# Optimization experiments

Measured on AMD Instinct MI355X. Metric: run time of the kernel, lower is better.

Reference implementation:

```python
import jax, jax.numpy as jnp
import numpy as np

K = 7          # kernel_size
PAD = 3        # padding
GROUPS = 8
OUTC = 128
INC = 128
REFINE = True


def conv1x1(x, w):
    # x: [B,C,H,W], w: [O,C] (1x1 conv, no bias)
    return jnp.einsum('oc,bchw->bohw', w, x)


def unfold2d(x, k):
    # x: [B,C,Hp,Wp] -> [B,C,h,w,k,k], stride 1 (matches torch unfold(2,k).unfold(3,k))
    B, C, Hp, Wp = x.shape
    h, w = Hp - k + 1, Wp - k + 1
    patches = jnp.stack([x[:, :, i:i + h, j:j + w] for i in range(k) for j in range(k)], axis=-1)
    return patches.reshape(B, C, h, w, k, k)


def unfold1d(x, k, axis):
    # sliding window of size k, stride 1, along axis 2 (rows) or 3 (cols)
    if axis == 2:
        h = x.shape[2] - k + 1
        return jnp.stack([x[:, :, i:i + h, :] for i in range(k)], axis=-1)  # [B,C,h,W,k]
    else:
        w = x.shape[3] - k + 1
        return jnp.stack([x[:, :, :, j:j + w] for j in range(k)], axis=-1)  # [B,C,H,w,k]


def _forward(feature_map, wq, wk, wv, rel_h, rel_w):
    c = feature_map.shape[1] // 2
    fm_t0, fm_t1 = feature_map[:, :c], feature_map[:, c:]
    B, _, H, W = fm_t0.shape
    cg = OUTC // GROUPS

    padded_t0 = jnp.pad(fm_t0, ((0, 0), (0, 0), (PAD, PAD), (PAD, PAD)))
    q = conv1x1(fm_t1, wq)                 # [B,OUTC,H,W]
    k_full = conv1x1(padded_t0, wk)        # [B,OUTC,H+2p,W+2p]
    v_full = conv1x1(padded_t0, wv)

    k_win = unfold2d(k_full, K)            # [B,OUTC,H,W,K,K]
    k_h, k_w = k_win[:, :OUTC // 2], k_win[:, OUTC // 2:]
    k_win = jnp.concatenate([k_h + rel_h, k_w + rel_w], axis=1)
    k_win = k_win.reshape(B, GROUPS, cg, H, W, K * K)
    v_win = unfold2d(v_full, K).reshape(B, GROUPS, cg, H, W, K * K)

    qg = q.reshape(B, GROUPS, cg, H, W, 1)
    attn = jax.nn.softmax(jnp.sum(qg * k_win, axis=2), axis=-1)  # [B,G,H,W,K*K]
    out = jnp.einsum('bnhwk,bnchwk->bnchw', attn, v_win).reshape(B, OUTC, H, W)

    if REFINE:
        win = 2 * K + 1
        p_col = jnp.pad(fm_t0, ((0, 0), (0, 0), (K, K), (0, 0)))
        p_row = jnp.pad(fm_t0, ((0, 0), (0, 0), (0, 0), (K, K)))
        k_col = unfold1d(conv1x1(p_col, wk), win, 2).reshape(B, GROUPS, cg, H, W, win)
        k_row = unfold1d(conv1x1(p_row, wk), win, 3).reshape(B, GROUPS, cg, H, W, win)
        v_col = unfold1d(conv1x1(p_col, wv), win, 2).reshape(B, GROUPS, cg, H, W, win)
        v_row = unfold1d(conv1x1(p_row, wv), win, 3).reshape(B, GROUPS, cg, H, W, win)

        a_row = jax.nn.softmax(jnp.sum(qg * k_row, axis=2), axis=-1)
        a_col = jax.nn.softmax(jnp.sum(qg * k_col, axis=2), axis=-1)
        out = out + jnp.einsum('bnhwk,bnchwk->bnchw', a_row, v_row).reshape(B, OUTC, H, W)
        out = out + jnp.einsum('bnhwk,bnchwk->bnchw', a_col, v_col).reshape(B, OUTC, H, W)
    return out


def setup_inputs() -> dict:
    key = jax.random.key(0)
    ks = jax.random.split(key, 6)
    B, H, W = 2, 64, 64
    feature_map = jax.random.normal(ks[0], (B, 2 * INC, H, W), dtype=jnp.float32)
    # kaiming_normal fan_out for 1x1 conv: std = sqrt(2 / outc)
    std = float(np.sqrt(2.0 / OUTC))
    wq = jax.random.normal(ks[1], (OUTC, INC), dtype=jnp.float32) * std
    wk = jax.random.normal(ks[2], (OUTC, INC), dtype=jnp.float32) * std
    wv = jax.random.normal(ks[3], (OUTC, INC), dtype=jnp.float32) * std
    rel_h = jax.random.normal(ks[4], (OUTC // 2, 1, 1, K, 1), dtype=jnp.float32)
    rel_w = jax.random.normal(ks[5], (OUTC // 2, 1, 1, 1, K), dtype=jnp.float32)
    return {"feature_map": feature_map, "wq": wq, "wk": wk, "wv": wv,
            "rel_h": rel_h, "rel_w": rel_w}


def reference(feature_map, wq, wk, wv, rel_h, rel_w):
    return _forward(feature_map, wq, wk, wv, rel_h, rel_w)
```

## Files before the change

### kernel.cpp

```cpp
#include <hip/hip_runtime.h>
#include <hip/hip_bf16.h>

__device__ __forceinline__ float bf2f(unsigned short u) {
    union { unsigned int i; float f; } v; v.i = ((unsigned int)u) << 16; return v.f;
}
__device__ __forceinline__ unsigned short f2bf(float f) {
    __hip_bfloat16 h = __float2bfloat16(f);
    return *reinterpret_cast<unsigned short*>(&h);
}


#define CANVAS_SLAB 102400

__device__ __forceinline__ void zero_pad_slice(
    unsigned short* __restrict__ C, int blockId, int tid)
{
    const int slab = blockId >> 4;
    const int part = blockId & 15;
    unsigned short* base = C + (size_t)slab * CANVAS_SLAB;
    #pragma unroll
    for (int r = 0; r < 2; ++r) {
        const int t = tid + r * 256;
        if (t < 288) {
            const int u    = part * 288 + t;
            const int cell = u >> 1;
            const int half = u & 1;
            int row, col;
            if (cell < 640)       { row = cell / 80;  col = cell - row * 80; }
            else if (cell < 1280) { const int c2 = cell - 640;  const int rr = c2 / 80;
                                    row = 72 + rr;  col = c2 - rr * 80; }
            else if (cell < 1792) { const int c2 = cell - 1280;
                                    row = 8 + (c2 >> 3);  col = c2 & 7; }
            else                  { const int c2 = cell - 1792;
                                    row = 8 + (c2 >> 3);  col = 72 + (c2 & 7); }
            *(uint4*)(base + (size_t)(row * 80 + col) * 16 + half * 8) =
                make_uint4(0u, 0u, 0u, 0u);
        }
    }
}

__global__ __launch_bounds__(256) void conv_kernel(
    const float* __restrict__ fm,
    const float* __restrict__ wq, const float* __restrict__ wk,
    const float* __restrict__ wv,
    float* __restrict__ Qout,
    unsigned short* __restrict__ K0,
    unsigned short* __restrict__ V0)
{
    const int sel = blockIdx.z;
    const int by  = blockIdx.y;
    const float* W = (sel == 0) ? wq : ((sel == 1) ? wk : wv);
    const int c0 = (sel == 0) ? 128 : 0;

    __shared__ float w_s[64 * 68];
    __shared__ float x_s[64 * 68];

    const int tid = threadIdx.x;
    const int P0  = blockIdx.x * 64;
    const int b   = P0 >> 12;
    const int hw0 = P0 & 4095;

    if (sel == 1) zero_pad_slice(K0, blockIdx.x * 2 + by, tid);
    else if (sel == 2) zero_pad_slice(V0, blockIdx.x * 2 + by, tid);

    float acc[4][4];
    #pragma unroll
    for (int i = 0; i < 4; ++i)
        #pragma unroll
        for (int j = 0; j < 4; ++j) acc[i][j] = 0.f;

    const int ocb = (tid >> 4) * 4;
    const int pxb = (tid & 15) * 4;

    for (int kh = 0; kh < 128; kh += 64) {
        {
            const int o    = tid >> 2;
            const int koff = (tid & 3) * 16;
            #pragma unroll
            for (int i = 0; i < 4; ++i) {
                float4 v = *(const float4*)(W + (size_t)(by * 64 + o) * 128 + kh + koff + i * 4);
                w_s[(koff + i * 4 + 0) * 68 + o] = v.x;
                w_s[(koff + i * 4 + 1) * 68 + o] = v.y;
                w_s[(koff + i * 4 + 2) * 68 + o] = v.z;
                w_s[(koff + i * 4 + 3) * 68 + o] = v.w;
            }
        }
        {
            const int c  = tid >> 2;
            const int pc = (tid & 3) * 16;
            const float* src = fm + (((size_t)(b * 256 + c0 + kh + c)) << 12) + hw0 + pc;
            #pragma unroll
            for (int i = 0; i < 4; ++i)
                *(float4*)(&x_s[c * 68 + pc + i * 4]) = *(const float4*)(src + i * 4);
        }
        __syncthreads();
        #pragma unroll 8
        for (int k = 0; k < 64; ++k) {
            float4 wa = *(const float4*)(&w_s[k * 68 + ocb]);
            float4 xv = *(const float4*)(&x_s[k * 68 + pxb]);
            const float wf[4] = {wa.x, wa.y, wa.z, wa.w};
            const float xf[4] = {xv.x, xv.y, xv.z, xv.w};
            #pragma unroll
            for (int i = 0; i < 4; ++i)
                #pragma unroll
                for (int j = 0; j < 4; ++j) acc[i][j] += wf[i] * xf[j];
        }
        __syncthreads();
    }

    const int oc  = by * 64 + ocb;
    const int g   = oc >> 4;
    const int lci = oc & 15;
    const int hh  = hw0 >> 6;
    #pragma unroll
    for (int pj = 0; pj < 4; ++pj) {
        const int ww = pxb + pj;
        if (sel == 0) {
            const size_t base = ((((size_t)(b * 8 + g)) << 12) + (hh * 64 + ww)) * 16 + lci;
            *(float4*)(Qout + base) = make_float4(acc[0][pj], acc[1][pj], acc[2][pj], acc[3][pj]);
        } else {
            const size_t cbase = (size_t)(b * 8 + g) * CANVAS_SLAB
                               + ((size_t)((hh + 8) * 80 + (ww + 8))) * 16 + lci;
            unsigned short tmp[4];
            #pragma unroll
            for (int i = 0; i < 4; ++i) tmp[i] = f2bf(acc[i][pj]);
            unsigned short* dst = ((sel == 1) ? K0 : V0) + cbase;
            *(uint2*)dst = *(const uint2*)tmp;
        }
    }
}

struct KV16 { uint4 a, b; };
__device__ __forceinline__ KV16 ld16(const unsigned short* p) {
    KV16 r; r.a = *(const uint4*)p; r.b = *(const uint4*)(p + 8); return r;
}
__device__ __forceinline__ float dotq(const float* q, const KV16& k) {
    const unsigned short* u = (const unsigned short*)&k;
    float s = 0.f;
    #pragma unroll
    for (int c = 0; c < 16; ++c) s += q[c] * bf2f(u[c]);
    return s;
}
__device__ __forceinline__ void axpyq(float* acc, float wgt, const KV16& v) {
    const unsigned short* u = (const unsigned short*)&v;
    #pragma unroll
    for (int c = 0; c < 16; ++c) acc[c] += wgt * bf2f(u[c]);
}

#define CIDX(y, x) (((size_t)(((y) + 8) * 80 + ((x) + 8))) << 4)

template<int I0, int NI>
__device__ __forceinline__ void main_chunk(
    const float* qr, const unsigned short* Kp, const unsigned short* Vp,
    const float* __restrict__ rel_h, const float* __restrict__ rel_w,
    int g, int h, int w, float* acc, float& mx, float& den)
{
    float qrel[7];
    const float* rel = (g < 4) ? (rel_h + g * 112) : (rel_w + (g - 4) * 112);
    #pragma unroll
    for (int t = 0; t < 7; ++t) {
        float s = 0.f;
        #pragma unroll
        for (int ci = 0; ci < 16; ++ci) s += qr[ci] * rel[ci * 7 + t];
        qrel[t] = s;
    }
    const bool bias_i = (g < 4);

    float sc[NI * 7];
    mx = -3.4e38f;
    #pragma unroll
    for (int i = 0; i < NI; ++i) {
        const int y = h + (I0 + i) - 3;
        #pragma unroll
        for (int j = 0; j < 7; ++j) {
            const int x = w + j - 3;
            float d = dotq(qr, ld16(Kp + CIDX(y, x)));
            d += bias_i ? qrel[I0 + i] : qrel[j];
            sc[i * 7 + j] = d;
            mx = fmaxf(mx, d);
        }
    }
    den = 0.f;
    #pragma unroll
    for (int k = 0; k < NI * 7; ++k) { sc[k] = __expf(sc[k] - mx); den += sc[k]; }
    #pragma unroll
    for (int i = 0; i < NI; ++i) {
        const int y = h + (I0 + i) - 3;
        #pragma unroll
        for (int j = 0; j < 7; ++j) {
            const int x = w + j - 3;
            axpyq(acc, sc[i * 7 + j], ld16(Vp + CIDX(y, x)));
        }
    }
}

__global__ __launch_bounds__(256) void attn_kernel(
    const float* __restrict__ Q,
    const unsigned short* __restrict__ K0,
    const unsigned short* __restrict__ V0,
    const float* __restrict__ rel_h,
    const float* __restrict__ rel_w,
    float* __restrict__ ACC,
    float* __restrict__ Mb,
    float* __restrict__ Db)
{
    const int tid = threadIdx.x;
    const int id  = blockIdx.x;
    const int s   = id & 15;
    const int j   = id >> 4;
    const int xt  = j & 15;
    const int pz  = j >> 4;
    const int b   = s >> 3;
    const int g   = s & 7;
    const int w   = tid & 63;
    const int h   = xt * 4 + (tid >> 6);

    const size_t slabQ = ((size_t)s) << 16;
    const float* qptr = Q + slabQ + (size_t)(h * 64 + w) * 16;

    float qr[16];
    #pragma unroll
    for (int ci = 0; ci < 16; ++ci) qr[ci] = qptr[ci];

    const unsigned short* Kp = K0 + (size_t)s * CANVAS_SLAB;
    const unsigned short* Vp = V0 + (size_t)s * CANVAS_SLAB;

    float acc[16];
    #pragma unroll
    for (int ci = 0; ci < 16; ++ci) acc[ci] = 0.f;
    float mx, den;

    if (pz == 0) {
        main_chunk<4, 3>(qr, Kp, Vp, rel_h, rel_w, g, h, w, acc, mx, den);
    } else if (pz == 1) {
        main_chunk<0, 2>(qr, Kp, Vp, rel_h, rel_w, g, h, w, acc, mx, den);
    } else if (pz == 2) {
        main_chunk<2, 2>(qr, Kp, Vp, rel_h, rel_w, g, h, w, acc, mx, den);
    } else if (pz == 3) {
        float sc[15];
        mx = -3.4e38f;
        #pragma unroll
        for (int jj = 0; jj < 15; ++jj) {
            const int x = w + jj - 7;
            const float d = dotq(qr, ld16(Kp + CIDX(h, x)));
            sc[jj] = d; mx = fmaxf(mx, d);
        }
        den = 0.f;
        #pragma unroll
        for (int jj = 0; jj < 15; ++jj) { sc[jj] = __expf(sc[jj] - mx); den += sc[jj]; }
        #pragma unroll
        for (int jj = 0; jj < 15; ++jj) {
            const int x = w + jj - 7;
            axpyq(acc, sc[jj], ld16(Vp + CIDX(h, x)));
        }
    } else {
        float sc[15];
        mx = -3.4e38f;
        #pragma unroll
        for (int i = 0; i < 15; ++i) {
            const int y = h + i - 7;
            const float d = dotq(qr, ld16(Kp + CIDX(y, w)));
            sc[i] = d; mx = fmaxf(mx, d);
        }
        den = 0.f;
        #pragma unroll
        for (int i = 0; i < 15; ++i) { sc[i] = __expf(sc[i] - mx); den += sc[i]; }
        #pragma unroll
        for (int i = 0; i < 15; ++i) {
            const int y = h + i - 7;
            axpyq(acc, sc[i], ld16(Vp + CIDX(y, w)));
        }
    }

    const int hw = h * 64 + w;
    float* op = ACC + ((((size_t)(pz * 2 + b)) * 128 + g * 16) << 12) + hw;
    #pragma unroll
    for (int ci = 0; ci < 16; ++ci)
        op[(size_t)ci << 12] = acc[ci];
    const size_t md = ((((size_t)(pz * 2 + b)) * 8 + g) << 12) + hw;
    Mb[md] = mx;
    Db[md] = den;
}
#undef CIDX

__global__ __launch_bounds__(256) void combine_kernel(
    const float4* __restrict__ ACC,
    const float* __restrict__ Mb, const float* __restrict__ Db,
    float4* __restrict__ out)
{
    const int idx = blockIdx.x * 256 + threadIdx.x;
    const int i4  = idx & 1023;
    const int ch  = (idx >> 10) & 127;
    const int b   = idx >> 17;
    const int g   = ch >> 4;

    const float4* M4 = (const float4*)Mb;
    const float4* D4 = (const float4*)Db;

    float4 A[5], Mv[3], Dv[5];
    #pragma unroll
    for (int p = 0; p < 5; ++p) {
        A[p]  = ACC[(((size_t)(p * 2 + b) * 128 + ch) << 10) + i4];
        Dv[p] = D4[(((size_t)(p * 2 + b) * 8 + g) << 10) + i4];
    }
    #pragma unroll
    for (int p = 0; p < 3; ++p)
        Mv[p] = M4[(((size_t)(p * 2 + b) * 8 + g) << 10) + i4];

    const float* a0 = (const float*)&A[0]; const float* a1 = (const float*)&A[1];
    const float* a2 = (const float*)&A[2]; const float* a3 = (const float*)&A[3];
    const float* a4 = (const float*)&A[4];
    const float* m0 = (const float*)&Mv[0]; const float* m1 = (const float*)&Mv[1];
    const float* m2 = (const float*)&Mv[2];
    const float* d0 = (const float*)&Dv[0]; const float* d1 = (const float*)&Dv[1];
    const float* d2 = (const float*)&Dv[2]; const float* d3 = (const float*)&Dv[3];
    const float* d4 = (const float*)&Dv[4];

    float res[4];
    #pragma unroll
    for (int c = 0; c < 4; ++c) {
        const float M  = fmaxf(m0[c], fmaxf(m1[c], m2[c]));
        const float e0 = __expf(m0[c] - M);
        const float e1 = __expf(m1[c] - M);
        const float e2 = __expf(m2[c] - M);
        const float num = a0[c] * e0 + a1[c] * e1 + a2[c] * e2;
        const float den = d0[c] * e0 + d1[c] * e1 + d2[c] * e2;
        res[c] = num / den + a3[c] / d3[c] + a4[c] / d4[c];
    }
    out[idx] = make_float4(res[0], res[1], res[2], res[3]);
}

extern "C" void kernel_launch(void* const* d_in, const int* in_sizes, int n_in,
                              void* d_out, int out_size, void* d_ws, size_t ws_size,
                              hipStream_t stream) {
    (void)in_sizes; (void)n_in; (void)ws_size; (void)out_size;
    const float* fm    = (const float*)d_in[0];
    const float* wq    = (const float*)d_in[1];
    const float* wk    = (const float*)d_in[2];
    const float* wv    = (const float*)d_in[3];
    const float* rel_h = (const float*)d_in[4];
    const float* rel_w = (const float*)d_in[5];

    float* Q = (float*)d_ws;
    unsigned short* K0 = (unsigned short*)(Q + 1048576);
    unsigned short* V0 = K0 + 16 * CANVAS_SLAB;
    float* ACC = (float*)(V0 + 16 * CANVAS_SLAB);
    float* Mb  = ACC + 5242880;
    float* Db  = Mb + 327680;

    conv_kernel<<<dim3(128, 2, 3), dim3(256), 0, stream>>>(
        fm, wq, wk, wv, Q, K0, V0);
    attn_kernel<<<dim3(1280, 1, 1), dim3(256), 0, stream>>>(
        Q, K0, V0, rel_h, rel_w, ACC, Mb, Db);
    combine_kernel<<<dim3(1024), dim3(256), 0, stream>>>(
        (const float4*)ACC, Mb, Db, (float4*)d_out);
}
```

Before: 103.5 us.

## Compute two adjacent pixels per thread to share K/V window loads

Each thread of the attention kernel now handles two horizontally adjacent output pixels, so their overlapping K and V window loads are shared. In the horizontal window this takes 8 loads instead of 14 per row, and 16 instead of 30 for the 15-wide row window. The grid is halved, the block order is reshuffled so the long column-window slice launches first, and outputs are written as float2. Register pressure roughly doubles because of the duplicate q, accumulator and score arrays, and with half as many threads in flight latency hiding may suffer.

```diff
diff --git a/kernel.cpp b/kernel.cpp
--- a/kernel.cpp
+++ b/kernel.cpp
@@ -150,46 +150,61 @@
 #define CIDX(y, x) (((size_t)(((y) + 8) * 80 + ((x) + 8))) << 4)
 
 template<int I0, int NI>
-__device__ __forceinline__ void main_chunk(
-    const float* qr, const unsigned short* Kp, const unsigned short* Vp,
+__device__ __forceinline__ void main_chunk2(
+    const float* qr0, const float* qr1,
+    const unsigned short* Kp, const unsigned short* Vp,
     const float* __restrict__ rel_h, const float* __restrict__ rel_w,
-    int g, int h, int w, float* acc, float& mx, float& den)
-{
-    float qrel[7];
+    int g, int h, int w0,
+    float* acc0, float* acc1, float& mx0, float& mx1, float& den0, float& den1)
+{
+    float qrel0[7], qrel1[7];
     const float* rel = (g < 4) ? (rel_h + g * 112) : (rel_w + (g - 4) * 112);
     #pragma unroll
     for (int t = 0; t < 7; ++t) {
-        float s = 0.f;
-        #pragma unroll
-        for (int ci = 0; ci < 16; ++ci) s += qr[ci] * rel[ci * 7 + t];
-        qrel[t] = s;
+        float s0 = 0.f, s1 = 0.f;
+        #pragma unroll
+        for (int ci = 0; ci < 16; ++ci) {
+            s0 += qr0[ci] * rel[ci * 7 + t];
+            s1 += qr1[ci] * rel[ci * 7 + t];
+        }
+        qrel0[t] = s0; qrel1[t] = s1;
     }
     const bool bias_i = (g < 4);
 
-    float sc[NI * 7];
-    mx = -3.4e38f;
+    float sc0[NI * 7], sc1[NI * 7];
+    mx0 = -3.4e38f; mx1 = -3.4e38f;
     #pragma unroll
     for (int i = 0; i < NI; ++i) {
         const int y = h + (I0 + i) - 3;
         #pragma unroll
-        for (int j = 0; j < 7; ++j) {
-            const int x = w + j - 3;
-            float d = dotq(qr, ld16(Kp + CIDX(y, x)));
-            d += bias_i ? qrel[I0 + i] : qrel[j];
-            sc[i * 7 + j] = d;
-            mx = fmaxf(mx, d);
-        }
-    }
-    den = 0.f;
-    #pragma unroll
-    for (int k = 0; k < NI * 7; ++k) { sc[k] = __expf(sc[k] - mx); den += sc[k]; }
+        for (int c = 0; c < 8; ++c) {
+            const int x = w0 + c - 3;
+            KV16 kv = ld16(Kp + CIDX(y, x));
+            if (c < 7) {
+                float d = dotq(qr0, kv) + (bias_i ? qrel0[I0 + i] : qrel0[c]);
+                sc0[i * 7 + c] = d; mx0 = fmaxf(mx0, d);
+            }
+            if (c > 0) {
+                float d = dotq(qr1, kv) + (bias_i ? qrel1[I0 + i] : qrel1[c - 1]);
+                sc1[i * 7 + c - 1] = d; mx1 = fmaxf(mx1, d);
+            }
+        }
+    }
+    den0 = 0.f; den1 = 0.f;
+    #pragma unroll
+    for (int k = 0; k < NI * 7; ++k) {
+        sc0[k] = __expf(sc0[k] - mx0); den0 += sc0[k];
+        sc1[k] = __expf(sc1[k] - mx1); den1 += sc1[k];
+    }
     #pragma unroll
     for (int i = 0; i < NI; ++i) {
         const int y = h + (I0 + i) - 3;
         #pragma unroll
-        for (int j = 0; j < 7; ++j) {
-            const int x = w + j - 3;
-            axpyq(acc, sc[i * 7 + j], ld16(Vp + CIDX(y, x)));
+        for (int c = 0; c < 8; ++c) {
+            const int x = w0 + c - 3;
+            KV16 kv = ld16(Vp + CIDX(y, x));
+            if (c < 7) axpyq(acc0, sc0[i * 7 + c], kv);
+            if (c > 0) axpyq(acc1, sc1[i * 7 + c - 1], kv);
         }
     }
 }
@@ -204,82 +219,97 @@
     float* __restrict__ Mb,
     float* __restrict__ Db)
 {
-    const int tid = threadIdx.x;
-    const int id  = blockIdx.x;
-    const int s   = id & 15;
-    const int j   = id >> 4;
-    const int xt  = j & 15;
-    const int pz  = j >> 4;
-    const int b   = s >> 3;
-    const int g   = s & 7;
-    const int w   = tid & 63;
-    const int h   = xt * 4 + (tid >> 6);
+    const int tid  = threadIdx.x;
+    const int id   = blockIdx.x;
+    const int s    = id & 15;
+    const int j    = id >> 4;
+    const int xt   = j & 7;
+    const int slot = j >> 3;
+    const int pz   = (slot == 0) ? 4 : slot - 1;
+    const int b    = s >> 3;
+    const int g    = s & 7;
+    const int w0   = (tid & 31) * 2;
+    const int h    = xt * 8 + (tid >> 5);
 
     const size_t slabQ = ((size_t)s) << 16;
-    const float* qptr = Q + slabQ + (size_t)(h * 64 + w) * 16;
-
-    float qr[16];
-    #pragma unroll
-    for (int ci = 0; ci < 16; ++ci) qr[ci] = qptr[ci];
+    const float* qptr = Q + slabQ + (size_t)(h * 64 + w0) * 16;
+
+    float qr0[16], qr1[16];
+    #pragma unroll
+    for (int ci = 0; ci < 16; ++ci) { qr0[ci] = qptr[ci]; qr1[ci] = qptr[16 + ci]; }
 
     const unsigned short* Kp = K0 + (size_t)s * CANVAS_SLAB;
     const unsigned short* Vp = V0 + (size_t)s * CANVAS_SLAB;
 
-    float acc[16];
-    #pragma unroll
-    for (int ci = 0; ci < 16; ++ci) acc[ci] = 0.f;
-    float mx, den;
+    float acc0[16], acc1[16];
+    #pragma unroll
+    for (int ci = 0; ci < 16; ++ci) { acc0[ci] = 0.f; acc1[ci] = 0.f; }
+    float mx0, mx1, den0, den1;
 
     if (pz == 0) {
-        main_chunk<4, 3>(qr, Kp, Vp, rel_h, rel_w, g, h, w, acc, mx, den);
+        main_chunk2<4, 3>(qr0, qr1, Kp, Vp, rel_h, rel_w, g, h, w0,
+                          acc0, acc1, mx0, mx1, den0, den1);
     } else if (pz == 1) {
-        main_chunk<0, 2>(qr, Kp, Vp, rel_h, rel_w, g, h, w, acc, mx, den);
+        main_chunk2<0, 2>(qr0, qr1, Kp, Vp, rel_h, rel_w, g, h, w0,
+                          acc0, acc1, mx0, mx1, den0, den1);
     } else if (pz == 2) {
-        main_chunk<2, 2>(qr, Kp, Vp, rel_h, rel_w, g, h, w, acc, mx, den);
+        main_chunk2<2, 2>(qr0, qr1, Kp, Vp, rel_h, rel_w, g, h, w0,
+                          acc0, acc1, mx0, mx1, den0, den1);
     } else if (pz == 3) {
-        float sc[15];
-        mx = -3.4e38f;
-        #pragma unroll
-        for (int jj = 0; jj < 15; ++jj) {
-            const int x = w + jj - 7;
-            const float d = dotq(qr, ld16(Kp + CIDX(h, x)));
-            sc[jj] = d; mx = fmaxf(mx, d);
-        }
-        den = 0.f;
-        #pragma unroll
-        for (int jj = 0; jj < 15; ++jj) { sc[jj] = __expf(sc[jj] - mx); den += sc[jj]; }
-        #pragma unroll
-        for (int jj = 0; jj < 15; ++jj) {
-            const int x = w + jj - 7;
-            axpyq(acc, sc[jj], ld16(Vp + CIDX(h, x)));
+        float sc0[15], sc1[15];
+        mx0 = -3.4e38f; mx1 = -3.4e38f;
+        #pragma unroll
+        for (int c = 0; c < 16; ++c) {
+            const int x = w0 + c - 7;
+            KV16 kv = ld16(Kp + CIDX(h, x));
+            if (c < 15) { sc0[c] = dotq(qr0, kv); mx0 = fmaxf(mx0, sc0[c]); }
+            if (c > 0)  { sc1[c - 1] = dotq(qr1, kv); mx1 = fmaxf(mx1, sc1[c - 1]); }
+        }
+        den0 = 0.f; den1 = 0.f;
+        #pragma unroll
+        for (int k = 0; k < 15; ++k) {
+            sc0[k] = __expf(sc0[k] - mx0); den0 += sc0[k];
+            sc1[k] = __expf(sc1[k] - mx1); den1 += sc1[k];
+        }
+        #pragma unroll
+        for (int c = 0; c < 16; ++c) {
+            const int x = w0 + c - 7;
+            KV16 kv = ld16(Vp + CIDX(h, x));
+            if (c < 15) axpyq(acc0, sc0[c], kv);
+            if (c > 0)  axpyq(acc1, sc1[c - 1], kv);
         }
     } else {
-        float sc[15];
-        mx = -3.4e38f;
+        float sc0[15], sc1[15];
+        mx0 = -3.4e38f; mx1 = -3.4e38f;
         #pragma unroll
         for (int i = 0; i < 15; ++i) {
             const int y = h + i - 7;
-            const float d = dotq(qr, ld16(Kp + CIDX(y, w)));
-            sc[i] = d; mx = fmaxf(mx, d);
-        }
-        den = 0.f;
-        #pragma unroll
-        for (int i = 0; i < 15; ++i) { sc[i] = __expf(sc[i] - mx); den += sc[i]; }
+            sc0[i] = dotq(qr0, ld16(Kp + CIDX(y, w0)));
+            sc1[i] = dotq(qr1, ld16(Kp + CIDX(y, w0 + 1)));
+            mx0 = fmaxf(mx0, sc0[i]); mx1 = fmaxf(mx1, sc1[i]);
+        }
+        den0 = 0.f; den1 = 0.f;
+        #pragma unroll
+        for (int i = 0; i < 15; ++i) {
+            sc0[i] = __expf(sc0[i] - mx0); den0 += sc0[i];
+            sc1[i] = __expf(sc1[i] - mx1); den1 += sc1[i];
+        }
         #pragma unroll
         for (int i = 0; i < 15; ++i) {
             const int y = h + i - 7;
-            axpyq(acc, sc[i], ld16(Vp + CIDX(y, w)));
-        }
-    }
-
-    const int hw = h * 64 + w;
+            axpyq(acc0, sc0[i], ld16(Vp + CIDX(y, w0)));
+            axpyq(acc1, sc1[i], ld16(Vp + CIDX(y, w0 + 1)));
+        }
+    }
+
+    const int hw = h * 64 + w0;
     float* op = ACC + ((((size_t)(pz * 2 + b)) * 128 + g * 16) << 12) + hw;
     #pragma unroll
     for (int ci = 0; ci < 16; ++ci)
-        op[(size_t)ci << 12] = acc[ci];
+        *(float2*)(op + ((size_t)ci << 12)) = make_float2(acc0[ci], acc1[ci]);
     const size_t md = ((((size_t)(pz * 2 + b)) * 8 + g) << 12) + hw;
-    Mb[md] = mx;
-    Db[md] = den;
+    *(float2*)(Mb + md) = make_float2(mx0, mx1);
+    *(float2*)(Db + md) = make_float2(den0, den1);
 }
 #undef CIDX
 
@@ -350,7 +380,7 @@
 
     conv_kernel<<<dim3(128, 2, 3), dim3(256), 0, stream>>>(
         fm, wq, wk, wv, Q, K0, V0);
-    attn_kernel<<<dim3(1280, 1, 1), dim3(256), 0, stream>>>(
+    attn_kernel<<<dim3(640, 1, 1), dim3(256), 0, stream>>>(
         Q, K0, V0, rel_h, rel_w, ACC, Mb, Db);
     combine_kernel<<<dim3(1024), dim3(256), 0, stream>>>(
         (const float4*)ACC, Mb, Db, (float4*)d_out);
```

Result: slower. 113.3 us (+9.5%).
